# Kernel tuning notes

Hardware: AMD Instinct MI355X
Metric: run time of the kernel (lower is better)

## Reference

```python
import jax, jax.numpy as jnp
import numpy as np

N_NODES = 50000
N_EDGES = 1600000
SLOPE = 0.01  # torch leaky_relu default negative_slope


def _lrelu(x):
    return jnp.where(x >= 0, x, SLOPE * x)


def _graph_conv(x, edge_index, w_rel, b_rel, w_root):
    # PyG GraphConv (aggr='add'): out_i = W_rel @ sum_{j->i} x_j + b_rel + W_root @ x_i
    src, dst = edge_index[0], edge_index[1]
    agg = jax.ops.segment_sum(x[src], dst, num_segments=x.shape[0])  # [N, F_in]
    return agg @ w_rel.T + b_rel + x @ w_root.T


def setup_inputs() -> dict:
    key = jax.random.key(0)
    ks = jax.random.split(key, 12)

    def glorot(k, shape):
        fan_in = shape[-1]
        return jax.random.normal(k, shape, dtype=jnp.float32) / np.sqrt(fan_in)

    x = jax.random.normal(ks[0], (N_NODES, 2048), dtype=jnp.float32)
    edge_index = jax.random.randint(ks[1], (2, N_EDGES), 0, N_NODES, dtype=jnp.int64)

    return {
        "x": x,
        "edge_index": edge_index,
        "lin1_w": glorot(ks[2], (128, 2048)),
        "lin1_b": jnp.zeros((128,), jnp.float32),
        "conv1_w_rel": glorot(ks[3], (64, 128)),
        "conv1_b_rel": jnp.zeros((64,), jnp.float32),
        "conv1_w_root": glorot(ks[4], (64, 128)),
        "conv4_w_rel": glorot(ks[5], (32, 64)),
        "conv4_b_rel": jnp.zeros((32,), jnp.float32),
        "conv4_w_root": glorot(ks[6], (32, 64)),
        "pos_w": glorot(ks[7], (3, 32)),
        "pos_b": jnp.zeros((3,), jnp.float32),
    }


def reference(x, edge_index, lin1_w, lin1_b, conv1_w_rel, conv1_b_rel,
              conv1_w_root, conv4_w_rel, conv4_b_rel, conv4_w_root,
              pos_w, pos_b):
    # dropout layers are identity at inference
    h = _lrelu(x @ lin1_w.T + lin1_b)                                  # [N, 128]
    h = _lrelu(_graph_conv(h, edge_index, conv1_w_rel, conv1_b_rel, conv1_w_root))  # [N, 64]
    h = _lrelu(_graph_conv(h, edge_index, conv4_w_rel, conv4_b_rel, conv4_w_root))  # [N, 32]
    position = h @ pos_w.T + pos_b                                     # [N, 3]
    return position
```

## Files before the change

### kernel.cpp

```cpp
#include <hip/hip_runtime.h>

#define N_NODES 50000
#define N_EDGES 1600000

typedef __attribute__((ext_vector_type(4))) float f32x4;
typedef __attribute__((ext_vector_type(8))) short bf16x8;
typedef unsigned short u16;

__device__ __forceinline__ float lrelu(float x) { return x >= 0.f ? x : 0.01f * x; }

__device__ __forceinline__ u16 f2bf(float f) {
    union { float f; unsigned u; } v; v.f = f;
    unsigned u = v.u;
    u += 0x7fffu + ((u >> 16) & 1u);
    return (u16)(u >> 16);
}

__device__ __forceinline__ float bf2f(u16 v) {
    union { unsigned u; float f; } x; x.u = ((unsigned)v) << 16; return x.f;
}

__device__ __forceinline__ bf16x8 cvt8(float4 a, float4 b) {
    bf16x8 r;
    r[0] = (short)f2bf(a.x); r[1] = (short)f2bf(a.y);
    r[2] = (short)f2bf(a.z); r[3] = (short)f2bf(a.w);
    r[4] = (short)f2bf(b.x); r[5] = (short)f2bf(b.y);
    r[6] = (short)f2bf(b.z); r[7] = (short)f2bf(b.w);
    return r;
}

__device__ __forceinline__ void gload_lds16(const void* g, void* l) {
    __builtin_amdgcn_global_load_lds(
        (const __attribute__((address_space(1))) void*)g,
        (__attribute__((address_space(3))) void*)l, 16, 0, 0);
}

__launch_bounds__(256)
__global__ void k_prep(const float* __restrict__ W1,
                       const float* __restrict__ W2a, const float* __restrict__ W2b,
                       const float* __restrict__ W3a, const float* __restrict__ W3b,
                       u16* __restrict__ wf1, u16* __restrict__ wf2, u16* __restrict__ wf3,
                       int* __restrict__ deg)
{
    const int b = blockIdx.x;
    if (b < 1024) {
        int i = b * 256 + threadIdx.x;
        int e = i & 7, lane = (i >> 3) & 63, nf = (i >> 9) & 7, ks = i >> 12;
        int n = nf * 16 + (lane & 15);
        int k = ks * 32 + 8 * (lane >> 4) + e;
        wf1[i] = f2bf(W1[(size_t)n * 2048 + k]);
    } else if (b < 1088) {
        int i = (b - 1024) * 256 + threadIdx.x;
        int e = i & 7, lane = (i >> 3) & 63, nf = (i >> 9) & 7, ks = i >> 12;
        int n = nf * 16 + (lane & 15);
        int k = ks * 32 + 8 * (lane >> 4) + e;
        float v = (n < 64) ? W2a[(size_t)n * 128 + k] : W2b[(size_t)(n - 64) * 128 + k];
        wf2[i] = f2bf(v);
    } else if (b < 1104) {
        int i = (b - 1088) * 256 + threadIdx.x;
        int e = i & 7, lane = (i >> 3) & 63, nf = (i >> 9) & 3, ks = i >> 11;
        int n = nf * 16 + (lane & 15);
        int k = ks * 32 + 8 * (lane >> 4) + e;
        float v = (n < 32) ? W3a[(size_t)n * 64 + k] : W3b[(size_t)(n - 32) * 64 + k];
        wf3[i] = f2bf(v);
    } else {
        int i = (b - 1104) * 256 + threadIdx.x;
        if (i < N_NODES) deg[i] = 0;
    }
}

__device__ __forceinline__ void stage_step(const float* __restrict__ X,
                                           const u16* __restrict__ Wf,
                                           char* slot, int m0, int s, int t)
{
    const int wave = t >> 6, l = t & 63;
    const int j = l >> 3, g = l & 7;
#pragma unroll
    for (int r = 0; r < 2; r++) {
        int lrow = r * 32 + wave * 8 + j;
        int grow = m0 + lrow; if (grow >= N_NODES) grow = N_NODES - 1;
        const float* srcA = X + (size_t)grow * 2048 + s * 32 + (((g ^ j) * 16) >> 2);
        gload_lds16(srcA, slot + r * 4096 + wave * 1024);
    }
#pragma unroll
    for (int r = 0; r < 2; r++) {
        const u16* srcB = Wf + (size_t)s * 4096 + (size_t)(r * 256 + t) * 8;
        gload_lds16(srcB, slot + 8192 + r * 4096 + wave * 1024);
    }
}

__device__ __forceinline__ void compute_step(const char* slot, int lane, int wave,
                                             f32x4 acc[8])
{
    const int lrow = lane & 15, lgrp = lane >> 4;
    const int row = wave * 16 + lrow;
    const int swz = (row & 7) << 4;
    const char* Ab = slot + row * 128;
    float4 a0 = *(const float4*)(Ab + ((lgrp * 32) ^ swz));
    float4 a1 = *(const float4*)(Ab + ((lgrp * 32 + 16) ^ swz));
    bf16x8 af = cvt8(a0, a1);
    const char* Bb = slot + 8192 + lane * 16;
    __builtin_amdgcn_s_setprio(1);
#pragma unroll
    for (int nf = 0; nf < 8; nf++) {
        bf16x8 bf = *(const bf16x8*)(Bb + nf * 1024);
        acc[nf] = __builtin_amdgcn_mfma_f32_16x16x32_bf16(af, bf, acc[nf], 0, 0, 0);
    }
    __builtin_amdgcn_s_setprio(0);
}

__launch_bounds__(256, 3)
__global__ void k_lin1d(const float* __restrict__ X, const u16* __restrict__ Wf1,
                        const u16* __restrict__ Wf2,
                        const float* __restrict__ Bv, const float* __restrict__ brel,
                        u16* __restrict__ t1, float* __restrict__ acc1)
{
    __shared__ __align__(16) char lds[3][16384];
    const int t = threadIdx.x, wave = t >> 6, lane = t & 63;
    const int lrow = lane & 15, lgrp = lane >> 4;
    const int m0 = blockIdx.x * 64;

    f32x4 acc[8];
#pragma unroll
    for (int i = 0; i < 8; i++) acc[i] = (f32x4)0.f;

    stage_step(X, Wf1, lds[0], m0, 0, t);
    stage_step(X, Wf1, lds[1], m0, 1, t);
    stage_step(X, Wf1, lds[2], m0, 2, t);

    for (int s = 0; s < 61; s++) {
        asm volatile("s_waitcnt vmcnt(8)" ::: "memory");
        __builtin_amdgcn_s_barrier();
        compute_step(lds[0] + (s % 3) * 16384, lane, wave, acc);
        __builtin_amdgcn_s_barrier();
        stage_step(X, Wf1, lds[0] + (s % 3) * 16384, m0, s + 3, t);
    }
    asm volatile("s_waitcnt vmcnt(8)" ::: "memory");
    __builtin_amdgcn_s_barrier();
    compute_step(lds[1], lane, wave, acc);
    asm volatile("s_waitcnt vmcnt(4)" ::: "memory");
    __builtin_amdgcn_s_barrier();
    compute_step(lds[2], lane, wave, acc);
    asm volatile("s_waitcnt vmcnt(0)" ::: "memory");
    __builtin_amdgcn_s_barrier();
    compute_step(lds[0], lane, wave, acc);

    u16* hl = (u16*)(lds[1] + wave * 4096);
#pragma unroll
    for (int nf = 0; nf < 8; nf++) {
        const int col = nf * 16 + lrow;
        const float bias = Bv[col];
#pragma unroll
        for (int r = 0; r < 4; r++) {
            const int row = lgrp * 4 + r;
            hl[row * 128 + (((col >> 3) ^ (row & 7)) << 3) + (col & 7)] =
                f2bf(lrelu(acc[nf][r] + bias));
        }
    }
    bf16x8 af2[4];
#pragma unroll
    for (int ks = 0; ks < 4; ks++)
        af2[ks] = *(const bf16x8*)(hl + lrow * 128 + ((((ks << 2) + lgrp) ^ (lrow & 7)) << 3));

    f32x4 dacc[8];
#pragma unroll
    for (int i = 0; i < 8; i++) dacc[i] = (f32x4)0.f;
    const u16* bp2 = Wf2 + lane * 8;
#pragma unroll
    for (int ks = 0; ks < 4; ks++) {
#pragma unroll
        for (int nf = 0; nf < 8; nf++) {
            bf16x8 bf = *(const bf16x8*)(bp2 + ks * 4096 + nf * 512);
            dacc[nf] = __builtin_amdgcn_mfma_f32_16x16x32_bf16(af2[ks], bf, dacc[nf], 0, 0, 0);
        }
    }

    const int rbase = m0 + wave * 16 + lgrp * 4;
#pragma unroll
    for (int nf = 0; nf < 8; nf++) {
        const int col = nf * 16 + lrow;
#pragma unroll
        for (int r = 0; r < 4; r++) {
            const int row = rbase + r;
            if (row < N_NODES) {
                if (col < 64) t1[(size_t)row * 64 + col] = f2bf(dacc[nf][r]);
                else          acc1[(size_t)row * 64 + (col - 64)] = dacc[nf][r] + brel[col - 64];
            }
        }
    }
}

__launch_bounds__(256, 2)
__global__ void k_dualf2(const float* __restrict__ A, const u16* __restrict__ Wf,
                         const float* __restrict__ brel,
                         u16* __restrict__ t2, float* __restrict__ acc2)
{
    const int t = threadIdx.x, wave = t >> 6, lane = t & 63;
    const int lrow = lane & 15, lgrp = lane >> 4;
    const int arow = blockIdx.x * 64 + wave * 16 + lrow;
    const float* ap = A + (size_t)(arow < N_NODES ? arow : 0) * 64 + 8 * lgrp;
    const u16* bp = Wf + lane * 8;

    float4 a00 = *(const float4*)(ap + 0);
    float4 a01 = *(const float4*)(ap + 4);
    float4 a10 = *(const float4*)(ap + 32);
    float4 a11 = *(const float4*)(ap + 36);

    f32x4 acc[4];
#pragma unroll
    for (int i = 0; i < 4; i++) acc[i] = (f32x4)0.f;

    a00.x = lrelu(a00.x); a00.y = lrelu(a00.y); a00.z = lrelu(a00.z); a00.w = lrelu(a00.w);
    a01.x = lrelu(a01.x); a01.y = lrelu(a01.y); a01.z = lrelu(a01.z); a01.w = lrelu(a01.w);
    bf16x8 af0 = cvt8(a00, a01);
    a10.x = lrelu(a10.x); a10.y = lrelu(a10.y); a10.z = lrelu(a10.z); a10.w = lrelu(a10.w);
    a11.x = lrelu(a11.x); a11.y = lrelu(a11.y); a11.z = lrelu(a11.z); a11.w = lrelu(a11.w);
    bf16x8 af1 = cvt8(a10, a11);

#pragma unroll
    for (int nf = 0; nf < 4; nf++) {
        bf16x8 b0 = *(const bf16x8*)(bp + nf * 512);
        bf16x8 b1 = *(const bf16x8*)(bp + 2048 + nf * 512);
        acc[nf] = __builtin_amdgcn_mfma_f32_16x16x32_bf16(af0, b0, acc[nf], 0, 0, 0);
        acc[nf] = __builtin_amdgcn_mfma_f32_16x16x32_bf16(af1, b1, acc[nf], 0, 0, 0);
    }

    const int rbase = blockIdx.x * 64 + wave * 16 + lgrp * 4;
#pragma unroll
    for (int nf = 0; nf < 4; nf++) {
        const int col = nf * 16 + lrow;
#pragma unroll
        for (int r = 0; r < 4; r++) {
            const int row = rbase + r;
            if (row < N_NODES) {
                if (col < 32) t2[(size_t)row * 32 + col] = f2bf(acc[nf][r]);
                else          acc2[(size_t)row * 32 + (col - 32)] = acc[nf][r] + brel[col - 32];
            }
        }
    }
}

__launch_bounds__(256)
__global__ void k_hist(const int* __restrict__ ei, int* __restrict__ deg)
{
    const int stride = gridDim.x * 256;
    for (int e = blockIdx.x * 256 + threadIdx.x; e < N_EDGES; e += stride)
        atomicAdd(deg + ei[N_EDGES + e], 1);
}

__launch_bounds__(256)
__global__ void k_scan1(const int* __restrict__ deg, int* __restrict__ tmp,
                        int* __restrict__ bsum)
{
    __shared__ int sm[256];
    const int tid = threadIdx.x;
    const int i = blockIdx.x * 256 + tid;
    int d = (i < N_NODES) ? deg[i] : 0;
    sm[tid] = d;
    __syncthreads();
#pragma unroll
    for (int off = 1; off < 256; off <<= 1) {
        int v = (tid >= off) ? sm[tid - off] : 0;
        __syncthreads();
        sm[tid] += v;
        __syncthreads();
    }
    if (i < N_NODES) tmp[i] = sm[tid];
    if (tid == 255) bsum[blockIdx.x] = sm[255];
}

__launch_bounds__(256)
__global__ void k_scan2p(const int* __restrict__ bsum, int* __restrict__ boff, int nb)
{
    __shared__ int sm[256];
    const int tid = threadIdx.x;
    int v = (tid < nb) ? bsum[tid] : 0;
    sm[tid] = v;
    __syncthreads();
#pragma unroll
    for (int off = 1; off < 256; off <<= 1) {
        int u = (tid >= off) ? sm[tid - off] : 0;
        __syncthreads();
        sm[tid] += u;
        __syncthreads();
    }
    if (tid < nb) boff[tid] = sm[tid] - v;
}

__launch_bounds__(256)
__global__ void k_scan3(const int* __restrict__ tmp, const int* __restrict__ boff,
                        const int* __restrict__ deg, int* __restrict__ ro,
                        int* __restrict__ cur)
{
    const int i = blockIdx.x * 256 + threadIdx.x;
    if (i < N_NODES) {
        int incl = tmp[i] + boff[i >> 8];
        ro[i + 1] = incl;
        cur[i] = incl - deg[i];
    }
    if (i == 0) ro[0] = 0;
}

__launch_bounds__(256)
__global__ void k_fill(const int* __restrict__ ei, int* __restrict__ cur,
                       int* __restrict__ csr)
{
    const int stride = gridDim.x * 256;
    for (int e = blockIdx.x * 256 + threadIdx.x; e < N_EDGES; e += stride) {
        const int dst = ei[N_EDGES + e];
        const int p = atomicAdd(cur + dst, 1);
        csr[p] = ei[e];
    }
}

__launch_bounds__(256)
__global__ void k_gather64(const int* __restrict__ ro, const int* __restrict__ csr,
                           const u16* __restrict__ t, float* __restrict__ acc)
{
    const int wid = (blockIdx.x << 2) | (threadIdx.x >> 6);
    if (wid >= N_NODES) return;
    const int lane = threadIdx.x & 63;
    const int s = ro[wid], e = ro[wid + 1];
    float a = acc[(size_t)wid * 64 + lane];
    int i = s;
    for (; i + 8 <= e; i += 8) {
        int s0 = csr[i], s1 = csr[i + 1], s2 = csr[i + 2], s3 = csr[i + 3];
        int s4 = csr[i + 4], s5 = csr[i + 5], s6 = csr[i + 6], s7 = csr[i + 7];
        u16 v0 = t[(size_t)s0 * 64 + lane], v1 = t[(size_t)s1 * 64 + lane];
        u16 v2 = t[(size_t)s2 * 64 + lane], v3 = t[(size_t)s3 * 64 + lane];
        u16 v4 = t[(size_t)s4 * 64 + lane], v5 = t[(size_t)s5 * 64 + lane];
        u16 v6 = t[(size_t)s6 * 64 + lane], v7 = t[(size_t)s7 * 64 + lane];
        a += bf2f(v0); a += bf2f(v1); a += bf2f(v2); a += bf2f(v3);
        a += bf2f(v4); a += bf2f(v5); a += bf2f(v6); a += bf2f(v7);
    }
    for (; i < e; ++i) a += bf2f(t[(size_t)csr[i] * 64 + lane]);
    acc[(size_t)wid * 64 + lane] = a;
}

__launch_bounds__(256)
__global__ void k_gpos(const int* __restrict__ ro, const int* __restrict__ csr,
                       const u16* __restrict__ t, const float* __restrict__ acc2,
                       const float* __restrict__ PW, const float* __restrict__ PB,
                       float* __restrict__ out)
{
    const int wid = (blockIdx.x << 2) | (threadIdx.x >> 6);
    if (wid >= N_NODES) return;
    const int lane = threadIdx.x & 63;
    const int half = lane >> 5, f = lane & 31;
    const int s = ro[wid], e = ro[wid + 1];
    float a = 0.f;
    int i = s;
    for (; i + 8 <= e; i += 8) {
        int s0 = csr[i + half], s1 = csr[i + 2 + half];
        int s2 = csr[i + 4 + half], s3 = csr[i + 6 + half];
        u16 v0 = t[(size_t)s0 * 32 + f], v1 = t[(size_t)s1 * 32 + f];
        u16 v2 = t[(size_t)s2 * 32 + f], v3 = t[(size_t)s3 * 32 + f];
        a += bf2f(v0); a += bf2f(v1); a += bf2f(v2); a += bf2f(v3);
    }
    for (; i < e; i += 2) {
        int idx = i + half;
        if (idx < e) a += bf2f(t[(size_t)csr[idx] * 32 + f]);
    }
    a += __shfl_xor(a, 32, 64);

    float v = lrelu(acc2[(size_t)wid * 32 + f] + a);
    float p0 = v * PW[f], p1 = v * PW[32 + f], p2 = v * PW[64 + f];
#pragma unroll
    for (int off = 16; off >= 1; off >>= 1) {
        p0 += __shfl_xor(p0, off, 64);
        p1 += __shfl_xor(p1, off, 64);
        p2 += __shfl_xor(p2, off, 64);
    }
    if (lane == 0) {
        out[(size_t)wid * 3 + 0] = p0 + PB[0];
        out[(size_t)wid * 3 + 1] = p1 + PB[1];
        out[(size_t)wid * 3 + 2] = p2 + PB[2];
    }
}

extern "C" void kernel_launch(void* const* d_in, const int* in_sizes, int n_in,
                              void* d_out, int out_size, void* d_ws, size_t ws_size,
                              hipStream_t stream)
{
    const float* x        = (const float*)d_in[0];
    const int*   ei       = (const int*)d_in[1];
    const float* lin1_w   = (const float*)d_in[2];
    const float* lin1_b   = (const float*)d_in[3];
    const float* c1_wrel  = (const float*)d_in[4];
    const float* c1_brel  = (const float*)d_in[5];
    const float* c1_wroot = (const float*)d_in[6];
    const float* c4_wrel  = (const float*)d_in[7];
    const float* c4_brel  = (const float*)d_in[8];
    const float* c4_wroot = (const float*)d_in[9];
    const float* pos_w    = (const float*)d_in[10];
    const float* pos_b    = (const float*)d_in[11];
    float* out = (float*)d_out;

    char* base = (char*)d_ws;
    u16*   t1b  = (u16*)base;
    float* acc1 = (float*)(base + 6400000);
    u16*   t2b  = (u16*)(base + 19200000);
    float* acc2 = (float*)(base + 22400000);
    u16*   wf1  = (u16*)(base + 28800000);
    u16*   wf2  = wf1 + 262144;
    u16*   wf3  = wf2 + 16384;
    int*   ibase = (int*)(wf3 + 4096);
    const int NPAD = ((N_NODES + 255) / 256) * 256;
    int* deg  = ibase;
    int* tmp  = deg  + NPAD;
    int* ro   = tmp  + NPAD;
    int* cur  = ro   + NPAD;
    int* bsum = cur  + NPAD;
    int* boff = bsum + 256;
    int* csr  = boff + 256;
    const int NB = (N_NODES + 255) / 256;

    hipLaunchKernelGGL(k_prep, dim3(1104 + NB), dim3(256), 0, stream,
                       lin1_w, c1_wrel, c1_wroot, c4_wrel, c4_wroot,
                       wf1, wf2, wf3, deg);
    hipLaunchKernelGGL(k_hist, dim3(2048), dim3(256), 0, stream, ei, deg);
    hipLaunchKernelGGL(k_scan1, dim3(NB), dim3(256), 0, stream, deg, tmp, bsum);
    hipLaunchKernelGGL(k_scan2p, dim3(1), dim3(256), 0, stream, bsum, boff, NB);
    hipLaunchKernelGGL(k_scan3, dim3(NB), dim3(256), 0, stream, tmp, boff, deg, ro, cur);
    hipLaunchKernelGGL(k_fill, dim3(2048), dim3(256), 0, stream, ei, cur, csr);

    hipLaunchKernelGGL(k_lin1d, dim3((N_NODES + 63) / 64), dim3(256), 0, stream,
                       x, wf1, wf2, lin1_b, c1_brel, t1b, acc1);
    hipLaunchKernelGGL(k_gather64, dim3((N_NODES + 3) / 4), dim3(256), 0, stream,
                       ro, csr, t1b, acc1);
    hipLaunchKernelGGL(k_dualf2, dim3((N_NODES + 63) / 64), dim3(256), 0, stream,
                       acc1, wf3, c4_brel, t2b, acc2);
    hipLaunchKernelGGL(k_gpos, dim3((N_NODES + 3) / 4), dim3(256), 0, stream,
                       ro, csr, t2b, acc2, pos_w, pos_b, out);
}
```

Measured before the change: 441.0 us.

## Fuse histogram into prep and CSR fill into lin1 GEMM, register-staged double buffer

The degree histogram moves into the weight-prep kernel, with the degree array zeroed by a memset. The CSR fill loop is appended to the tail of the lin1 GEMM kernel so edge scatter overlaps GEMM work across blocks, removing two launches. The lin1 main loop drops the direct global-to-LDS async loads and the triple buffer. It now uses register prefetch two steps ahead, explicit LDS stores and a double buffer with two barriers per step. That trade may expose more load latency and costs extra VGPRs and LDS stores.

Result: faster. 369.7 us (-16.2%).

```diff
diff --git a/kernel.cpp b/kernel.cpp
--- a/kernel.cpp
+++ b/kernel.cpp
@@ -2,6 +2,8 @@
 
 #define N_NODES 50000
 #define N_EDGES 1600000
+#define LIN_BLOCKS 782
+#define HIST_BLOCKS 1024
 
 typedef __attribute__((ext_vector_type(4))) float f32x4;
 typedef __attribute__((ext_vector_type(8))) short bf16x8;
@@ -29,18 +31,12 @@
     return r;
 }
 
-__device__ __forceinline__ void gload_lds16(const void* g, void* l) {
-    __builtin_amdgcn_global_load_lds(
-        (const __attribute__((address_space(1))) void*)g,
-        (__attribute__((address_space(3))) void*)l, 16, 0, 0);
-}
-
 __launch_bounds__(256)
 __global__ void k_prep(const float* __restrict__ W1,
                        const float* __restrict__ W2a, const float* __restrict__ W2b,
                        const float* __restrict__ W3a, const float* __restrict__ W3b,
                        u16* __restrict__ wf1, u16* __restrict__ wf2, u16* __restrict__ wf3,
-                       int* __restrict__ deg)
+                       const int* __restrict__ ei, int* __restrict__ deg)
 {
     const int b = blockIdx.x;
     if (b < 1024) {
@@ -64,29 +60,18 @@
         float v = (n < 32) ? W3a[(size_t)n * 64 + k] : W3b[(size_t)(n - 32) * 64 + k];
         wf3[i] = f2bf(v);
     } else {
-        int i = (b - 1104) * 256 + threadIdx.x;
-        if (i < N_NODES) deg[i] = 0;
-    }
-}
-
-__device__ __forceinline__ void stage_step(const float* __restrict__ X,
-                                           const u16* __restrict__ Wf,
-                                           char* slot, int m0, int s, int t)
-{
-    const int wave = t >> 6, l = t & 63;
-    const int j = l >> 3, g = l & 7;
-#pragma unroll
-    for (int r = 0; r < 2; r++) {
-        int lrow = r * 32 + wave * 8 + j;
-        int grow = m0 + lrow; if (grow >= N_NODES) grow = N_NODES - 1;
-        const float* srcA = X + (size_t)grow * 2048 + s * 32 + (((g ^ j) * 16) >> 2);
-        gload_lds16(srcA, slot + r * 4096 + wave * 1024);
-    }
-#pragma unroll
-    for (int r = 0; r < 2; r++) {
-        const u16* srcB = Wf + (size_t)s * 4096 + (size_t)(r * 256 + t) * 8;
-        gload_lds16(srcB, slot + 8192 + r * 4096 + wave * 1024);
-    }
+        for (int e = (b - 1104) * 256 + threadIdx.x; e < N_EDGES; e += HIST_BLOCKS * 256)
+            atomicAdd(deg + ei[N_EDGES + e], 1);
+    }
+}
+
+__device__ __forceinline__ void wr_stage(char* slot, int aw0, int aw1, int bw,
+                                         float4 A0, float4 A1, float4 B0, float4 B1)
+{
+    *(float4*)(slot + aw0) = A0;
+    *(float4*)(slot + aw1) = A1;
+    *(float4*)(slot + bw) = B0;
+    *(float4*)(slot + bw + 16) = B1;
 }
 
 __device__ __forceinline__ void compute_step(const char* slot, int lane, int wave,
@@ -110,42 +95,67 @@
 }
 
 __launch_bounds__(256, 3)
-__global__ void k_lin1d(const float* __restrict__ X, const u16* __restrict__ Wf1,
-                        const u16* __restrict__ Wf2,
-                        const float* __restrict__ Bv, const float* __restrict__ brel,
-                        u16* __restrict__ t1, float* __restrict__ acc1)
-{
-    __shared__ __align__(16) char lds[3][16384];
+__global__ void k_linf(const float* __restrict__ X, const u16* __restrict__ Wf1,
+                       const u16* __restrict__ Wf2,
+                       const float* __restrict__ Bv, const float* __restrict__ brel,
+                       u16* __restrict__ t1, float* __restrict__ acc1,
+                       const int* __restrict__ ei, int* __restrict__ cur,
+                       int* __restrict__ csr)
+{
+    __shared__ __align__(16) char lds[2][16384];
+    __shared__ __align__(16) u16 hlbuf[4][2048];
+
     const int t = threadIdx.x, wave = t >> 6, lane = t & 63;
     const int lrow = lane & 15, lgrp = lane >> 4;
     const int m0 = blockIdx.x * 64;
 
+    const int arow_l = t >> 2, q = t & 3;
+    int grow = m0 + arow_l; if (grow >= N_NODES) grow = N_NODES - 1;
+    const float4* ap = (const float4*)(X + (size_t)grow * 2048);
+    const float4* bp = (const float4*)Wf1;
+    const int aw0 = arow_l * 128 + (((q * 2 + 0) ^ (arow_l & 7)) << 4);
+    const int aw1 = arow_l * 128 + (((q * 2 + 1) ^ (arow_l & 7)) << 4);
+    const int bw = 8192 + t * 32;
+
     f32x4 acc[8];
 #pragma unroll
     for (int i = 0; i < 8; i++) acc[i] = (f32x4)0.f;
 
-    stage_step(X, Wf1, lds[0], m0, 0, t);
-    stage_step(X, Wf1, lds[1], m0, 1, t);
-    stage_step(X, Wf1, lds[2], m0, 2, t);
-
-    for (int s = 0; s < 61; s++) {
-        asm volatile("s_waitcnt vmcnt(8)" ::: "memory");
+    float4 cA0 = ap[q * 2], cA1 = ap[q * 2 + 1];
+    float4 cB0 = bp[t * 2], cB1 = bp[t * 2 + 1];
+    float4 nA0 = ap[8 + q * 2], nA1 = ap[8 + q * 2 + 1];
+    float4 nB0 = bp[512 + t * 2], nB1 = bp[512 + t * 2 + 1];
+    wr_stage(lds[0], aw0, aw1, bw, cA0, cA1, cB0, cB1);
+    asm volatile("s_waitcnt lgkmcnt(0)" ::: "memory");
+    __builtin_amdgcn_s_barrier();
+    __builtin_amdgcn_sched_barrier(0);
+
+#pragma unroll 2
+    for (int s = 0; s < 62; s++) {
+        float4 fA0 = ap[(s + 2) * 8 + q * 2], fA1 = ap[(s + 2) * 8 + q * 2 + 1];
+        float4 fB0 = bp[(s + 2) * 512 + t * 2], fB1 = bp[(s + 2) * 512 + t * 2 + 1];
+
+        compute_step(lds[s & 1], lane, wave, acc);
         __builtin_amdgcn_s_barrier();
-        compute_step(lds[0] + (s % 3) * 16384, lane, wave, acc);
+        __builtin_amdgcn_sched_barrier(0);
+
+        wr_stage(lds[(s + 1) & 1], aw0, aw1, bw, nA0, nA1, nB0, nB1);
+        asm volatile("s_waitcnt lgkmcnt(0)" ::: "memory");
         __builtin_amdgcn_s_barrier();
-        stage_step(X, Wf1, lds[0] + (s % 3) * 16384, m0, s + 3, t);
-    }
-    asm volatile("s_waitcnt vmcnt(8)" ::: "memory");
+        __builtin_amdgcn_sched_barrier(0);
+
+        nA0 = fA0; nA1 = fA1; nB0 = fB0; nB1 = fB1;
+    }
+    compute_step(lds[0], lane, wave, acc);
     __builtin_amdgcn_s_barrier();
+    __builtin_amdgcn_sched_barrier(0);
+    wr_stage(lds[1], aw0, aw1, bw, nA0, nA1, nB0, nB1);
+    asm volatile("s_waitcnt lgkmcnt(0)" ::: "memory");
+    __builtin_amdgcn_s_barrier();
+    __builtin_amdgcn_sched_barrier(0);
     compute_step(lds[1], lane, wave, acc);
-    asm volatile("s_waitcnt vmcnt(4)" ::: "memory");
-    __builtin_amdgcn_s_barrier();
-    compute_step(lds[2], lane, wave, acc);
-    asm volatile("s_waitcnt vmcnt(0)" ::: "memory");
-    __builtin_amdgcn_s_barrier();
-    compute_step(lds[0], lane, wave, acc);
-
-    u16* hl = (u16*)(lds[1] + wave * 4096);
+
+    u16* hl = hlbuf[wave];
 #pragma unroll
     for (int nf = 0; nf < 8; nf++) {
         const int col = nf * 16 + lrow;
@@ -188,6 +198,12 @@
             }
         }
     }
+
+    for (int e = blockIdx.x * 256 + t; e < N_EDGES; e += LIN_BLOCKS * 256) {
+        const int dst = ei[N_EDGES + e];
+        const int p = atomicAdd(cur + dst, 1);
+        csr[p] = ei[e];
+    }
 }
 
 __launch_bounds__(256, 2)
@@ -241,14 +257,6 @@
 }
 
 __launch_bounds__(256)
-__global__ void k_hist(const int* __restrict__ ei, int* __restrict__ deg)
-{
-    const int stride = gridDim.x * 256;
-    for (int e = blockIdx.x * 256 + threadIdx.x; e < N_EDGES; e += stride)
-        atomicAdd(deg + ei[N_EDGES + e], 1);
-}
-
-__launch_bounds__(256)
 __global__ void k_scan1(const int* __restrict__ deg, int* __restrict__ tmp,
                         int* __restrict__ bsum)
 {
@@ -299,18 +307,6 @@
         cur[i] = incl - deg[i];
     }
     if (i == 0) ro[0] = 0;
-}
-
-__launch_bounds__(256)
-__global__ void k_fill(const int* __restrict__ ei, int* __restrict__ cur,
-                       int* __restrict__ csr)
-{
-    const int stride = gridDim.x * 256;
-    for (int e = blockIdx.x * 256 + threadIdx.x; e < N_EDGES; e += stride) {
-        const int dst = ei[N_EDGES + e];
-        const int p = atomicAdd(cur + dst, 1);
-        csr[p] = ei[e];
-    }
 }
 
 __launch_bounds__(256)
@@ -415,17 +411,16 @@
     int* csr  = boff + 256;
     const int NB = (N_NODES + 255) / 256;
 
-    hipLaunchKernelGGL(k_prep, dim3(1104 + NB), dim3(256), 0, stream,
+    hipMemsetAsync(deg, 0, (size_t)NPAD * sizeof(int), stream);
+    hipLaunchKernelGGL(k_prep, dim3(1104 + HIST_BLOCKS), dim3(256), 0, stream,
                        lin1_w, c1_wrel, c1_wroot, c4_wrel, c4_wroot,
-                       wf1, wf2, wf3, deg);
-    hipLaunchKernelGGL(k_hist, dim3(2048), dim3(256), 0, stream, ei, deg);
+                       wf1, wf2, wf3, ei, deg);
     hipLaunchKernelGGL(k_scan1, dim3(NB), dim3(256), 0, stream, deg, tmp, bsum);
     hipLaunchKernelGGL(k_scan2p, dim3(1), dim3(256), 0, stream, bsum, boff, NB);
     hipLaunchKernelGGL(k_scan3, dim3(NB), dim3(256), 0, stream, tmp, boff, deg, ro, cur);
-    hipLaunchKernelGGL(k_fill, dim3(2048), dim3(256), 0, stream, ei, cur, csr);
-
-    hipLaunchKernelGGL(k_lin1d, dim3((N_NODES + 63) / 64), dim3(256), 0, stream,
-                       x, wf1, wf2, lin1_b, c1_brel, t1b, acc1);
+
+    hipLaunchKernelGGL(k_linf, dim3(LIN_BLOCKS), dim3(256), 0, stream,
+                       x, wf1, wf2, lin1_b, c1_brel, t1b, acc1, ei, cur, csr);
     hipLaunchKernelGGL(k_gather64, dim3((N_NODES + 3) / 4), dim3(256), 0, stream,
                        ro, csr, t1b, acc1);
     hipLaunchKernelGGL(k_dualf2, dim3((N_NODES + 63) / 64), dim3(256), 0, stream,
```
